# Kernel tuning notes

Measured on AMD Instinct MI355X. Metric: run time of the kernel, lower is better.

## Reference

```python
import jax, jax.numpy as jnp
import numpy as np

N_ROI = 2000
N_CLASSES = 21            # VOC: 20 fg + background (class 0 skipped in suppression)
IMG_H, IMG_W = 600.0, 800.0
NMS_THRESH = 0.3          # use_preset('evaluate')
SCORE_THRESH = 0.05
LOC_MEAN = jnp.array([0.0, 0.0, 0.0, 0.0], jnp.float32)
LOC_STD = jnp.array([0.1, 0.1, 0.2, 0.2], jnp.float32)


def setup_inputs() -> dict:
    key = jax.random.key(0)
    k1, k2, k3, k4 = jax.random.split(key, 4)
    # rois in (y1, x1, y2, x2) with y2 > y1, x2 > x1, inside the image
    yx1 = jax.random.uniform(k1, (N_ROI, 2), jnp.float32) * jnp.array([IMG_H * 0.8, IMG_W * 0.8])
    hw = jax.random.uniform(k2, (N_ROI, 2), jnp.float32) * jnp.array([IMG_H * 0.3, IMG_W * 0.3]) + 8.0
    rois = jnp.concatenate([yx1, yx1 + hw], axis=1)
    roi_cls_locs = jax.random.normal(k3, (N_ROI, N_CLASSES * 4), jnp.float32) * 0.5
    roi_scores = jax.random.normal(k4, (N_ROI, N_CLASSES), jnp.float32) * 2.0
    scale = jnp.ones((1,), jnp.float32)
    return {"rois": rois, "roi_cls_locs": roi_cls_locs, "roi_scores": roi_scores, "scale": scale}


def loc2bbox(src_bbox, loc):
    # src_bbox, loc: [..., 4] in (y1, x1, y2, x2) / (dy, dx, dh, dw)
    h = src_bbox[..., 2] - src_bbox[..., 0]
    w = src_bbox[..., 3] - src_bbox[..., 1]
    cy = src_bbox[..., 0] + 0.5 * h
    cx = src_bbox[..., 1] + 0.5 * w
    dy, dx, dh, dw = loc[..., 0], loc[..., 1], loc[..., 2], loc[..., 3]
    ncy = dy * h + cy
    ncx = dx * w + cx
    nh = jnp.exp(dh) * h
    nw = jnp.exp(dw) * w
    return jnp.stack([ncy - 0.5 * nh, ncx - 0.5 * nw, ncy + 0.5 * nh, ncx + 0.5 * nw], axis=-1)


def pairwise_iou(b):
    # b: [N, 4] -> [N, N]
    area = (b[:, 2] - b[:, 0]) * (b[:, 3] - b[:, 1])
    ty = jnp.maximum(b[:, None, 0], b[None, :, 0])
    tx = jnp.maximum(b[:, None, 1], b[None, :, 1])
    by = jnp.minimum(b[:, None, 2], b[None, :, 2])
    bx = jnp.minimum(b[:, None, 3], b[None, :, 3])
    inter = jnp.clip(by - ty, 0.0) * jnp.clip(bx - tx, 0.0)
    return inter / (area[:, None] + area[None, :] - inter + 1e-12)


def nms_keep(boxes, scores, valid):
    # Fixed-shape NMS: returns boolean keep mask in original order.
    n = boxes.shape[0]
    order = jnp.argsort(-jnp.where(valid, scores, -jnp.inf))
    b = boxes[order]
    v = valid[order]
    iou = pairwise_iou(b)  # [N, N]
    idx = jnp.arange(n)

    def body(i, keep):
        sup = keep[i] & (iou[i] > NMS_THRESH) & (idx > i)
        return keep & ~sup

    keep_sorted = jax.lax.fori_loop(0, n, body, v)
    return jnp.zeros(n, bool).at[order].set(keep_sorted)


def reference(rois, roi_cls_locs, roi_scores, scale):
    n, c = roi_scores.shape
    mean = jnp.tile(LOC_MEAN, c)
    std = jnp.tile(LOC_STD, c)
    locs = (roi_cls_locs * std + mean).reshape(n, c, 4)
    src = jnp.broadcast_to(rois[:, None, :], (n, c, 4))
    bboxes = loc2bbox(src, locs)  # [N, C, 4]
    original_size = jnp.array([IMG_H, IMG_W], jnp.float32) / scale[0]
    bboxes = jnp.stack([
        jnp.clip(bboxes[..., 0], 0.0, original_size[0]),
        jnp.clip(bboxes[..., 1], 0.0, original_size[1]),
        jnp.clip(bboxes[..., 2], 0.0, original_size[0]),
        jnp.clip(bboxes[..., 3], 0.0, original_size[1]),
    ], axis=-1)
    prob = jax.nn.softmax(roi_scores, axis=-1)

    # drop background class 0; class-major layout [C-1, N, ...]
    boxes_c = jnp.transpose(bboxes[:, 1:, :], (1, 0, 2))  # [C-1, N, 4]
    probs_c = prob[:, 1:].T                                # [C-1, N]
    valid = probs_c > SCORE_THRESH
    keep = jax.vmap(nms_keep)(boxes_c, probs_c, valid)     # [C-1, N] bool

    out5 = jnp.where(keep[..., None],
                     jnp.concatenate([boxes_c, probs_c[..., None]], axis=-1),
                     0.0)                                  # [C-1, N, 5]
    labels = jnp.broadcast_to(jnp.arange(c - 1, dtype=jnp.int32)[:, None], keep.shape)
    return out5, keep, labels
```

## Files before the change

kernel.cpp:

```cpp
#include <hip/hip_runtime.h>
#include <math.h>

#define NROI 2000
#define NCLS 21
#define NFG  20
#define NPAD 2048
#define NTOT (NFG * NROI)

#define OFF_PROBS   0u
#define OFF_SIDX    160000u
#define OFF_SPROB   323840u
#define OFF_SBOX    487680u
#define OFF_VC      1143040u
#define OFF_MASK    1143296u

typedef unsigned long long u64;

__global__ void k_prob(const float* __restrict__ scores,
                       float* __restrict__ probs) {
#pragma clang fp contract(off)
    int n = blockIdx.x * blockDim.x + threadIdx.x;
    if (n >= NROI) return;
    float s[NCLS];
    float m = -__builtin_inff();
#pragma unroll
    for (int k = 0; k < NCLS; ++k) {
        s[k] = scores[n * NCLS + k];
        m = fmaxf(m, s[k]);
    }
    float sum = 0.0f;
#pragma unroll
    for (int k = 0; k < NCLS; ++k) sum += expf(s[k] - m);
#pragma unroll
    for (int c = 0; c < NFG; ++c)
        probs[c * NROI + n] = expf(s[c + 1] - m) / sum;
}

#define CSW(A,B,UP) { u64 lo_ = x[A] < x[B] ? x[A] : x[B]; \
                      u64 hi_ = x[A] < x[B] ? x[B] : x[A]; \
                      x[A] = (UP) ? lo_ : hi_; x[B] = (UP) ? hi_ : lo_; }

__global__ void __launch_bounds__(256) k_sort(const float* __restrict__ rois,
                                              const float* __restrict__ locs,
                                              const float* __restrict__ probs,
                                              const float* __restrict__ scale,
                                              int* __restrict__ sidx,
                                              float* __restrict__ sprob,
                                              float4* __restrict__ sbox,
                                              int* __restrict__ Vc,
                                              float* __restrict__ out) {
#pragma clang fp contract(off)
    int c = blockIdx.x;
    int cc = c + 1;
    int t = threadIdx.x;
    __shared__ u64 a[NPAD];
    __shared__ int vcount;
    if (t == 0) vcount = 0;

    u64 x[8];
    int cnt = 0;
#pragma unroll
    for (int i = 0; i < 8; ++i) {
        int e = 8 * t + i;
        unsigned int u;
        if (e < NROI) {
            float pr = probs[c * NROI + e];
            bool valid = pr > 0.05f;
            cnt += valid ? 1 : 0;
            float key = valid ? pr : -__builtin_inff();
            u = __float_as_uint(key);
        } else {
            u = __float_as_uint(-__builtin_inff());
        }
        u ^= (u >> 31) ? 0xFFFFFFFFu : 0x80000000u;
        x[i] = ((u64)(~u) << 32) | (unsigned int)e;
    }
    __syncthreads();
    if (cnt) atomicAdd(&vcount, cnt);

    {
        float4 z4 = make_float4(0.f, 0.f, 0.f, 0.f);
        float4* o5v = (float4*)out + (size_t)c * (NROI * 5 / 4);
        for (int i = t; i < NROI * 5 / 4; i += 256) o5v[i] = z4;
        float lc = (float)c;
        for (int i = t; i < NROI; i += 256) {
            out[(size_t)5 * NTOT + c * NROI + i] = 0.0f;
            out[(size_t)6 * NTOT + c * NROI + i] = lc;
        }
    }

    CSW(0,1,true)  CSW(2,3,false) CSW(4,5,true)  CSW(6,7,false)
    CSW(0,2,true)  CSW(1,3,true)  CSW(4,6,false) CSW(5,7,false)
    CSW(0,1,true)  CSW(2,3,true)  CSW(4,5,false) CSW(6,7,false)
    {
        bool up = (t & 1) == 0;
        CSW(0,4,up) CSW(1,5,up) CSW(2,6,up) CSW(3,7,up)
        CSW(0,2,up) CSW(1,3,up) CSW(4,6,up) CSW(5,7,up)
        CSW(0,1,up) CSW(2,3,up) CSW(4,5,up) CSW(6,7,up)
    }
    for (unsigned int k = 16; k <= NPAD; k <<= 1) {
        bool up = (((unsigned int)(8 * t)) & k) == 0;
        for (unsigned int j = k >> 1; j >= 8; j >>= 1) {
            if (j >= 512) {
                __syncthreads();
#pragma unroll
                for (int i = 0; i < 8; ++i) a[8 * t + i] = x[i];
                __syncthreads();
                bool lower = ((t & (j >> 3)) == 0);
                bool takeMin = (up == lower);
#pragma unroll
                for (int i = 0; i < 8; ++i) {
                    u64 y = a[(8 * t + i) ^ j];
                    u64 mn = x[i] < y ? x[i] : y;
                    u64 mx = x[i] < y ? y : x[i];
                    x[i] = takeMin ? mn : mx;
                }
            } else {
                int lm = (int)(j >> 3);
                bool lower = ((t & lm) == 0);
                bool takeMin = (up == lower);
#pragma unroll
                for (int i = 0; i < 8; ++i) {
                    u64 y = __shfl_xor(x[i], lm, 64);
                    u64 mn = x[i] < y ? x[i] : y;
                    u64 mx = x[i] < y ? y : x[i];
                    x[i] = takeMin ? mn : mx;
                }
            }
        }
        CSW(0,4,up) CSW(1,5,up) CSW(2,6,up) CSW(3,7,up)
        CSW(0,2,up) CSW(1,3,up) CSW(4,6,up) CSW(5,7,up)
        CSW(0,1,up) CSW(2,3,up) CSW(4,5,up) CSW(6,7,up)
    }

    float sc = scale[0];
    float oh = 600.0f / sc, ow = 800.0f / sc;
#pragma unroll
    for (int i = 0; i < 8; ++i) {
        int slot = 8 * t + i;
        u64 p = x[i];
        int orig = (int)(p & 0xFFFFFFFFu);
        sidx[c * NPAD + slot] = orig;
        unsigned int m_ = ~(unsigned int)(p >> 32);
        unsigned int b_ = (m_ & 0x80000000u) ? (m_ ^ 0x80000000u) : ~m_;
        sprob[c * NPAD + slot] = __uint_as_float(b_);

        float4 bb = make_float4(0.f, 0.f, 0.f, 0.f);
        if (orig < NROI) {
            const float4 rr = *(const float4*)(rois + (size_t)orig * 4);
            const float4 ll = *(const float4*)(locs + (size_t)orig * (NCLS * 4) + cc * 4);
            float h = rr.z - rr.x, w = rr.w - rr.y;
            float cy = rr.x + 0.5f * h, cx = rr.y + 0.5f * w;
            float dy = ll.x * 0.1f, dx = ll.y * 0.1f;
            float dh = ll.z * 0.2f, dw = ll.w * 0.2f;
            float ncy = dy * h + cy;
            float ncx = dx * w + cx;
            float nh = expf(dh) * h;
            float nw = expf(dw) * w;
            float b0 = ncy - 0.5f * nh;
            float b1 = ncx - 0.5f * nw;
            float b2 = ncy + 0.5f * nh;
            float b3 = ncx + 0.5f * nw;
            bb.x = fminf(fmaxf(b0, 0.0f), oh);
            bb.y = fminf(fmaxf(b1, 0.0f), ow);
            bb.z = fminf(fmaxf(b2, 0.0f), oh);
            bb.w = fminf(fmaxf(b3, 0.0f), ow);
        }
        sbox[c * NPAD + slot] = bb;
    }
    __syncthreads();
    if (t == 0) Vc[c] = vcount;
}

__global__ void __launch_bounds__(512) k_mask(const float4* __restrict__ sbox,
                                              const int* __restrict__ Vc,
                                              u64* __restrict__ mask) {
#pragma clang fp contract(off)
    int c = blockIdx.y;
    int V = Vc[c];
    int jb = blockIdx.x;
    int j0 = jb << 6;
    if (j0 >= V) return;
    int tid = threadIdx.x;
    int lane = tid & 63;
    int wv = tid >> 6;
    int rmax = min(V, j0 + 64);
    int smax = j0 + 64;

    __shared__ float4 lb[NPAD];
    const float4* sb = sbox + c * NPAD;
    for (int i = tid; i < smax; i += 512) lb[i] = sb[i];
    __syncthreads();

    int j = j0 + lane;
    float4 cb = lb[j];
    float areaC = (cb.z - cb.x) * (cb.w - cb.y);
    u64* mrow = mask + (size_t)(c * NPAD) * 32 + jb;

    for (int r0 = wv * 8; r0 < rmax; r0 += 64) {
#pragma unroll
        for (int k = 0; k < 8; ++k) {
            int r = r0 + k;
            bool act = r < rmax;
            float4 rb = lb[act ? r : 0];
            float areaR = (rb.z - rb.x) * (rb.w - rb.y);
            float ty = fmaxf(rb.x, cb.x);
            float tx = fmaxf(rb.y, cb.y);
            float by = fminf(rb.z, cb.z);
            float bx = fminf(rb.w, cb.w);
            float ih = fmaxf(by - ty, 0.0f);
            float iw = fmaxf(bx - tx, 0.0f);
            float inter = ih * iw;
            float denom = ((areaR + areaC) - inter) + 1e-12f;
            float iou = inter / denom;
            u64 bits = __ballot((j > r) && (iou > 0.3f));
            if (act && lane == 0) mrow[(size_t)r * 32] = bits;
        }
    }
}

__global__ void __launch_bounds__(64, 1) k_scan(const int* __restrict__ sidx,
                                                const float* __restrict__ sprob,
                                                const float4* __restrict__ sbox,
                                                const int* __restrict__ Vc,
                                                const u64* __restrict__ mask,
                                                float* __restrict__ out) {
    int c = blockIdx.x;
    int V = Vc[c];
    if (V <= 0) return;
    int lane = threadIdx.x;
    int w = lane & 31;
    const u64* mbase = mask + (size_t)c * NPAD * 32;

    int ntiles = (V + 63) >> 6;
    u64 remv = 0;
    u64 d = mbase[(size_t)lane * 32 + 0];

    for (int t = 0; t < ntiles; ++t) {
        u64 dn = 0;
        if (t + 1 < ntiles)
            dn = mbase[(size_t)(64 * (t + 1) + lane) * 32 + (t + 1)];

        int r = 64 * t + lane;
        bool act = r < V;
        int ri = act ? r : 0;
        int orig = sidx[c * NPAD + ri];
        float pr = sprob[c * NPAD + ri];
        float4 bb = sbox[c * NPAD + ri];

        u64 pf[64];
        const u64* rp = mbase + (size_t)(64 * t) * 32 + w;
#pragma unroll
        for (int j = 0; j < 64; ++j) pf[j] = rp[(size_t)j * 32];

        u64 rv = __shfl(remv, t);
        int rem = V - 64 * t;
        u64 validm = (rem >= 64) ? ~0ULL : ((1ULL << rem) - 1ULL);
        u64 cur = (~rv) & validm;
        u64 kept = 0;
        while (cur) {
            int j = __ffsll((u64)cur) - 1;
            kept |= 1ULL << j;
            cur &= ~__shfl(d, j);
            cur &= ~(1ULL << j);
        }

        u64 acc = 0;
#pragma unroll
        for (int j = 0; j < 64; ++j) {
            u64 sel = 0ULL - ((kept >> j) & 1ULL);
            acc |= pf[j] & sel;
        }
        remv |= acc;

        if (act && ((kept >> lane) & 1ULL)) {
            size_t to = (size_t)c * NROI + orig;
            float* o5 = out + to * 5;
            o5[0] = bb.x; o5[1] = bb.y; o5[2] = bb.z; o5[3] = bb.w; o5[4] = pr;
            out[(size_t)5 * NTOT + to] = 1.0f;
        }
        d = dn;
    }
}

extern "C" void kernel_launch(void* const* d_in, const int* in_sizes, int n_in,
                              void* d_out, int out_size, void* d_ws, size_t ws_size,
                              hipStream_t stream) {
    const float* rois   = (const float*)d_in[0];
    const float* locs   = (const float*)d_in[1];
    const float* scores = (const float*)d_in[2];
    const float* scale  = (const float*)d_in[3];
    float* out = (float*)d_out;

    char* ws = (char*)d_ws;
    float*  probs = (float*)(ws + OFF_PROBS);
    int*    sidx  = (int*)(ws + OFF_SIDX);
    float*  sprob = (float*)(ws + OFF_SPROB);
    float4* sbox  = (float4*)(ws + OFF_SBOX);
    int*    Vc    = (int*)(ws + OFF_VC);
    u64*    mask  = (u64*)(ws + OFF_MASK);

    hipLaunchKernelGGL(k_prob, dim3(32), dim3(64), 0, stream,
                       scores, probs);
    hipLaunchKernelGGL(k_sort, dim3(NFG), dim3(256), 0, stream,
                       rois, locs, probs, scale, sidx, sprob, sbox, Vc, out);
    hipLaunchKernelGGL(k_mask, dim3(32, NFG), dim3(512), 0, stream,
                       sbox, Vc, mask);
    hipLaunchKernelGGL(k_scan, dim3(NFG), dim3(64), 0, stream,
                       sidx, sprob, sbox, Vc, mask, out);
}
```

Before: 87.65 us.

## Fuse sort, IoU mask and NMS scan into one per-class kernel

Merges the sort, mask and scan kernels into a single 1024-thread block per class. Sorted keys and decoded boxes stay in LDS, and the IoU bitmask is stored as a packed upper triangle, in LDS when it fits and in global memory otherwise. This removes two launches and the global round trips for the sorted index, probability, box and mask buffers. The cost is that the mask computation now runs on only 20 workgroups instead of up to 640, so per-class parallelism drops, and the large LDS footprint allows one block per CU.

```diff
diff --git a/kernel.cpp b/kernel.cpp
--- a/kernel.cpp
+++ b/kernel.cpp
@@ -7,12 +7,12 @@
 #define NPAD 2048
 #define NTOT (NFG * NROI)
 
+#define NT_LDS_MAX 19
+#define TRI_LDS_WORDS 12160
+#define TRI_GBL_WORDS 33792
+
 #define OFF_PROBS   0u
-#define OFF_SIDX    160000u
-#define OFF_SPROB   323840u
-#define OFF_SBOX    487680u
-#define OFF_VC      1143040u
-#define OFF_MASK    1143296u
+#define OFF_GMASK   163840u
 
 typedef unsigned long long u64;
 
@@ -40,54 +40,53 @@
                       u64 hi_ = x[A] < x[B] ? x[B] : x[A]; \
                       x[A] = (UP) ? lo_ : hi_; x[B] = (UP) ? hi_ : lo_; }
 
-__global__ void __launch_bounds__(256) k_sort(const float* __restrict__ rois,
-                                              const float* __restrict__ locs,
-                                              const float* __restrict__ probs,
-                                              const float* __restrict__ scale,
-                                              int* __restrict__ sidx,
-                                              float* __restrict__ sprob,
-                                              float4* __restrict__ sbox,
-                                              int* __restrict__ Vc,
-                                              float* __restrict__ out) {
+__device__ __forceinline__ int tri_base(int T, int NT) {
+    return 64 * (T * NT - (T * (T - 1)) / 2);
+}
+
+__global__ void __launch_bounds__(1024, 1)
+k_mega(const float* __restrict__ rois,
+       const float* __restrict__ locs,
+       const float* __restrict__ probs,
+       const float* __restrict__ scale,
+       u64* __restrict__ gmask,
+       float* __restrict__ out) {
 #pragma clang fp contract(off)
     int c = blockIdx.x;
     int cc = c + 1;
     int t = threadIdx.x;
+
     __shared__ u64 a[NPAD];
+    __shared__ float4 lb[NPAD];
+    __shared__ u64 s_tri[TRI_LDS_WORDS];
     __shared__ int vcount;
     if (t == 0) vcount = 0;
 
     u64 x[8];
     int cnt = 0;
-#pragma unroll
-    for (int i = 0; i < 8; ++i) {
-        int e = 8 * t + i;
-        unsigned int u;
-        if (e < NROI) {
-            float pr = probs[c * NROI + e];
-            bool valid = pr > 0.05f;
-            cnt += valid ? 1 : 0;
-            float key = valid ? pr : -__builtin_inff();
-            u = __float_as_uint(key);
-        } else {
-            u = __float_as_uint(-__builtin_inff());
-        }
-        u ^= (u >> 31) ? 0xFFFFFFFFu : 0x80000000u;
-        x[i] = ((u64)(~u) << 32) | (unsigned int)e;
+    if (t < 256) {
+#pragma unroll
+        for (int i = 0; i < 8; ++i) {
+            int e = 8 * t + i;
+            unsigned int u;
+            if (e < NROI) {
+                float pr = probs[c * NROI + e];
+                bool valid = pr > 0.05f;
+                cnt += valid ? 1 : 0;
+                float key = valid ? pr : -__builtin_inff();
+                u = __float_as_uint(key);
+            } else {
+                u = __float_as_uint(-__builtin_inff());
+            }
+            u ^= (u >> 31) ? 0xFFFFFFFFu : 0x80000000u;
+            x[i] = ((u64)(~u) << 32) | (unsigned int)e;
+        }
+    } else {
+#pragma unroll
+        for (int i = 0; i < 8; ++i) x[i] = 0;
     }
     __syncthreads();
     if (cnt) atomicAdd(&vcount, cnt);
-
-    {
-        float4 z4 = make_float4(0.f, 0.f, 0.f, 0.f);
-        float4* o5v = (float4*)out + (size_t)c * (NROI * 5 / 4);
-        for (int i = t; i < NROI * 5 / 4; i += 256) o5v[i] = z4;
-        float lc = (float)c;
-        for (int i = t; i < NROI; i += 256) {
-            out[(size_t)5 * NTOT + c * NROI + i] = 0.0f;
-            out[(size_t)6 * NTOT + c * NROI + i] = lc;
-        }
-    }
 
     CSW(0,1,true)  CSW(2,3,false) CSW(4,5,true)  CSW(6,7,false)
     CSW(0,2,true)  CSW(1,3,true)  CSW(4,6,false) CSW(5,7,false)
@@ -103,17 +102,21 @@
         for (unsigned int j = k >> 1; j >= 8; j >>= 1) {
             if (j >= 512) {
                 __syncthreads();
-#pragma unroll
-                for (int i = 0; i < 8; ++i) a[8 * t + i] = x[i];
+                if (t < 256) {
+#pragma unroll
+                    for (int i = 0; i < 8; ++i) a[8 * t + i] = x[i];
+                }
                 __syncthreads();
-                bool lower = ((t & (j >> 3)) == 0);
-                bool takeMin = (up == lower);
-#pragma unroll
-                for (int i = 0; i < 8; ++i) {
-                    u64 y = a[(8 * t + i) ^ j];
-                    u64 mn = x[i] < y ? x[i] : y;
-                    u64 mx = x[i] < y ? y : x[i];
-                    x[i] = takeMin ? mn : mx;
+                if (t < 256) {
+                    bool lower = ((t & (j >> 3)) == 0);
+                    bool takeMin = (up == lower);
+#pragma unroll
+                    for (int i = 0; i < 8; ++i) {
+                        u64 y = a[(8 * t + i) ^ j];
+                        u64 mn = x[i] < y ? x[i] : y;
+                        u64 mx = x[i] < y ? y : x[i];
+                        x[i] = takeMin ? mn : mx;
+                    }
                 }
             } else {
                 int lm = (int)(j >> 3);
@@ -132,154 +135,147 @@
         CSW(0,2,up) CSW(1,3,up) CSW(4,6,up) CSW(5,7,up)
         CSW(0,1,up) CSW(2,3,up) CSW(4,5,up) CSW(6,7,up)
     }
-
-    float sc = scale[0];
-    float oh = 600.0f / sc, ow = 800.0f / sc;
-#pragma unroll
-    for (int i = 0; i < 8; ++i) {
-        int slot = 8 * t + i;
-        u64 p = x[i];
-        int orig = (int)(p & 0xFFFFFFFFu);
-        sidx[c * NPAD + slot] = orig;
-        unsigned int m_ = ~(unsigned int)(p >> 32);
-        unsigned int b_ = (m_ & 0x80000000u) ? (m_ ^ 0x80000000u) : ~m_;
-        sprob[c * NPAD + slot] = __uint_as_float(b_);
-
-        float4 bb = make_float4(0.f, 0.f, 0.f, 0.f);
-        if (orig < NROI) {
-            const float4 rr = *(const float4*)(rois + (size_t)orig * 4);
-            const float4 ll = *(const float4*)(locs + (size_t)orig * (NCLS * 4) + cc * 4);
-            float h = rr.z - rr.x, w = rr.w - rr.y;
-            float cy = rr.x + 0.5f * h, cx = rr.y + 0.5f * w;
-            float dy = ll.x * 0.1f, dx = ll.y * 0.1f;
-            float dh = ll.z * 0.2f, dw = ll.w * 0.2f;
-            float ncy = dy * h + cy;
-            float ncx = dx * w + cx;
-            float nh = expf(dh) * h;
-            float nw = expf(dw) * w;
-            float b0 = ncy - 0.5f * nh;
-            float b1 = ncx - 0.5f * nw;
-            float b2 = ncy + 0.5f * nh;
-            float b3 = ncx + 0.5f * nw;
-            bb.x = fminf(fmaxf(b0, 0.0f), oh);
-            bb.y = fminf(fmaxf(b1, 0.0f), ow);
-            bb.z = fminf(fmaxf(b2, 0.0f), oh);
-            bb.w = fminf(fmaxf(b3, 0.0f), ow);
-        }
-        sbox[c * NPAD + slot] = bb;
-    }
-    __syncthreads();
-    if (t == 0) Vc[c] = vcount;
-}
-
-__global__ void __launch_bounds__(512) k_mask(const float4* __restrict__ sbox,
-                                              const int* __restrict__ Vc,
-                                              u64* __restrict__ mask) {
-#pragma clang fp contract(off)
-    int c = blockIdx.y;
-    int V = Vc[c];
-    int jb = blockIdx.x;
-    int j0 = jb << 6;
-    if (j0 >= V) return;
-    int tid = threadIdx.x;
-    int lane = tid & 63;
-    int wv = tid >> 6;
-    int rmax = min(V, j0 + 64);
-    int smax = j0 + 64;
-
-    __shared__ float4 lb[NPAD];
-    const float4* sb = sbox + c * NPAD;
-    for (int i = tid; i < smax; i += 512) lb[i] = sb[i];
-    __syncthreads();
-
-    int j = j0 + lane;
-    float4 cb = lb[j];
-    float areaC = (cb.z - cb.x) * (cb.w - cb.y);
-    u64* mrow = mask + (size_t)(c * NPAD) * 32 + jb;
-
-    for (int r0 = wv * 8; r0 < rmax; r0 += 64) {
-#pragma unroll
-        for (int k = 0; k < 8; ++k) {
-            int r = r0 + k;
-            bool act = r < rmax;
-            float4 rb = lb[act ? r : 0];
-            float areaR = (rb.z - rb.x) * (rb.w - rb.y);
-            float ty = fmaxf(rb.x, cb.x);
-            float tx = fmaxf(rb.y, cb.y);
-            float by = fminf(rb.z, cb.z);
-            float bx = fminf(rb.w, cb.w);
-            float ih = fmaxf(by - ty, 0.0f);
-            float iw = fmaxf(bx - tx, 0.0f);
-            float inter = ih * iw;
-            float denom = ((areaR + areaC) - inter) + 1e-12f;
-            float iou = inter / denom;
-            u64 bits = __ballot((j > r) && (iou > 0.3f));
-            if (act && lane == 0) mrow[(size_t)r * 32] = bits;
-        }
-    }
-}
-
-__global__ void __launch_bounds__(64, 1) k_scan(const int* __restrict__ sidx,
-                                                const float* __restrict__ sprob,
-                                                const float4* __restrict__ sbox,
-                                                const int* __restrict__ Vc,
-                                                const u64* __restrict__ mask,
-                                                float* __restrict__ out) {
-    int c = blockIdx.x;
-    int V = Vc[c];
-    if (V <= 0) return;
-    int lane = threadIdx.x;
-    int w = lane & 31;
-    const u64* mbase = mask + (size_t)c * NPAD * 32;
-
-    int ntiles = (V + 63) >> 6;
-    u64 remv = 0;
-    u64 d = mbase[(size_t)lane * 32 + 0];
-
-    for (int t = 0; t < ntiles; ++t) {
-        u64 dn = 0;
-        if (t + 1 < ntiles)
-            dn = mbase[(size_t)(64 * (t + 1) + lane) * 32 + (t + 1)];
-
-        int r = 64 * t + lane;
-        bool act = r < V;
-        int ri = act ? r : 0;
-        int orig = sidx[c * NPAD + ri];
-        float pr = sprob[c * NPAD + ri];
-        float4 bb = sbox[c * NPAD + ri];
-
-        u64 pf[64];
-        const u64* rp = mbase + (size_t)(64 * t) * 32 + w;
-#pragma unroll
-        for (int j = 0; j < 64; ++j) pf[j] = rp[(size_t)j * 32];
-
-        u64 rv = __shfl(remv, t);
-        int rem = V - 64 * t;
-        u64 validm = (rem >= 64) ? ~0ULL : ((1ULL << rem) - 1ULL);
-        u64 cur = (~rv) & validm;
-        u64 kept = 0;
-        while (cur) {
-            int j = __ffsll((u64)cur) - 1;
-            kept |= 1ULL << j;
-            cur &= ~__shfl(d, j);
-            cur &= ~(1ULL << j);
-        }
-
-        u64 acc = 0;
-#pragma unroll
-        for (int j = 0; j < 64; ++j) {
-            u64 sel = 0ULL - ((kept >> j) & 1ULL);
-            acc |= pf[j] & sel;
-        }
-        remv |= acc;
-
-        if (act && ((kept >> lane) & 1ULL)) {
-            size_t to = (size_t)c * NROI + orig;
-            float* o5 = out + to * 5;
-            o5[0] = bb.x; o5[1] = bb.y; o5[2] = bb.z; o5[3] = bb.w; o5[4] = pr;
-            out[(size_t)5 * NTOT + to] = 1.0f;
-        }
-        d = dn;
+    __syncthreads();
+    if (t < 256) {
+#pragma unroll
+        for (int i = 0; i < 8; ++i) a[8 * t + i] = x[i];
+    }
+    __syncthreads();
+
+    int V = vcount;
+    int NT = (V + 63) >> 6;
+    bool use_lds = (NT <= NT_LDS_MAX);
+    u64* tri = use_lds ? (u64*)s_tri : (gmask + (size_t)c * TRI_GBL_WORDS);
+
+    {
+        float sc = scale[0];
+        float oh = 600.0f / sc, ow = 800.0f / sc;
+#pragma unroll
+        for (int q = 0; q < 2; ++q) {
+            int slot = t + q * 1024;
+            u64 p = a[slot];
+            int orig = (int)(p & 0xFFFFFFFFu);
+            float4 bb = make_float4(0.f, 0.f, 0.f, 0.f);
+            if (orig < NROI) {
+                const float4 rr = *(const float4*)(rois + (size_t)orig * 4);
+                const float4 ll = *(const float4*)(locs + (size_t)orig * (NCLS * 4) + cc * 4);
+                float h = rr.z - rr.x, w = rr.w - rr.y;
+                float cy = rr.x + 0.5f * h, cx = rr.y + 0.5f * w;
+                float dy = ll.x * 0.1f, dx = ll.y * 0.1f;
+                float dh = ll.z * 0.2f, dw = ll.w * 0.2f;
+                float ncy = dy * h + cy;
+                float ncx = dx * w + cx;
+                float nh = expf(dh) * h;
+                float nw = expf(dw) * w;
+                float b0 = ncy - 0.5f * nh;
+                float b1 = ncx - 0.5f * nw;
+                float b2 = ncy + 0.5f * nh;
+                float b3 = ncx + 0.5f * nw;
+                bb.x = fminf(fmaxf(b0, 0.0f), oh);
+                bb.y = fminf(fmaxf(b1, 0.0f), ow);
+                bb.z = fminf(fmaxf(b2, 0.0f), oh);
+                bb.w = fminf(fmaxf(b3, 0.0f), ow);
+            }
+            lb[slot] = bb;
+        }
+        float4 z4 = make_float4(0.f, 0.f, 0.f, 0.f);
+        float4* o5v = (float4*)out + (size_t)c * (NROI * 5 / 4);
+        for (int i = t; i < NROI * 5 / 4; i += 1024) o5v[i] = z4;
+        float lc = (float)c;
+        for (int i = t; i < NROI; i += 1024) {
+            out[(size_t)5 * NTOT + c * NROI + i] = 0.0f;
+            out[(size_t)6 * NTOT + c * NROI + i] = lc;
+        }
+    }
+    __syncthreads();
+
+    {
+        int lane = t & 63;
+        int wv = t >> 6;
+        int u = 0;
+        for (int rt = 0; rt < NT; ++rt) {
+            for (int jb = rt; jb < NT; ++jb, ++u) {
+                if ((u & 15) != wv) continue;
+                int j = (jb << 6) + lane;
+                float4 cb = lb[j];
+                float areaC = (cb.z - cb.x) * (cb.w - cb.y);
+                int r0 = rt << 6;
+                int rend = min(V, r0 + 64);
+                int stride = NT - rt;
+                int bidx = tri_base(rt, NT) + (jb - rt);
+#pragma unroll 4
+                for (int r = r0; r < rend; ++r) {
+                    float4 rb = lb[r];
+                    float areaR = (rb.z - rb.x) * (rb.w - rb.y);
+                    float ty = fmaxf(rb.x, cb.x);
+                    float tx = fmaxf(rb.y, cb.y);
+                    float by = fminf(rb.z, cb.z);
+                    float bx = fminf(rb.w, cb.w);
+                    float ih = fmaxf(by - ty, 0.0f);
+                    float iw = fmaxf(bx - tx, 0.0f);
+                    float inter = ih * iw;
+                    float denom = ((areaR + areaC) - inter) + 1e-12f;
+                    float iou = inter / denom;
+                    u64 bits = __ballot((j > r) && (iou > 0.3f));
+                    if (lane == 0) tri[bidx + (r - r0) * stride] = bits;
+                }
+            }
+        }
+    }
+    __syncthreads();
+
+    if (t < 64 && V > 0) {
+        int lane = t;
+        int w = lane & 31;
+        u64 remv = 0;
+        for (int T = 0; T < NT; ++T) {
+            int stride = NT - T;
+            int tb = tri_base(T, NT);
+            u64 d = tri[tb + lane * stride];
+
+            u64 rv = __shfl(remv, T);
+            int rem = V - 64 * T;
+            u64 validm = (rem >= 64) ? ~0ULL : ((1ULL << rem) - 1ULL);
+            u64 cur = (~rv) & validm;
+            u64 kept = 0;
+            while (cur) {
+                int j = __ffsll((u64)cur) - 1;
+                kept |= 1ULL << j;
+                cur &= ~__shfl(d, j);
+                cur &= ~(1ULL << j);
+            }
+
+            if (w >= T && w < NT) {
+                int bidx = tb + (w - T);
+                u64 acc = 0;
+#pragma unroll 1
+                for (int jj = 0; jj < 64; jj += 32) {
+                    u64 pf[32];
+#pragma unroll
+                    for (int q = 0; q < 32; ++q) pf[q] = tri[bidx + (jj + q) * stride];
+#pragma unroll
+                    for (int q = 0; q < 32; ++q) {
+                        u64 sel = 0ULL - ((kept >> (jj + q)) & 1ULL);
+                        acc |= pf[q] & sel;
+                    }
+                }
+                remv |= acc;
+            }
+
+            int r = 64 * T + lane;
+            if (r < V && ((kept >> lane) & 1ULL)) {
+                u64 p = a[r];
+                int orig = (int)(p & 0xFFFFFFFFu);
+                unsigned int m_ = ~(unsigned int)(p >> 32);
+                unsigned int b_ = (m_ & 0x80000000u) ? (m_ ^ 0x80000000u) : ~m_;
+                float pr = __uint_as_float(b_);
+                float4 bb = lb[r];
+                size_t to = (size_t)c * NROI + orig;
+                float* o5 = out + to * 5;
+                o5[0] = bb.x; o5[1] = bb.y; o5[2] = bb.z; o5[3] = bb.w; o5[4] = pr;
+                out[(size_t)5 * NTOT + to] = 1.0f;
+            }
+        }
     }
 }
 
@@ -293,19 +289,11 @@
     float* out = (float*)d_out;
 
     char* ws = (char*)d_ws;
-    float*  probs = (float*)(ws + OFF_PROBS);
-    int*    sidx  = (int*)(ws + OFF_SIDX);
-    float*  sprob = (float*)(ws + OFF_SPROB);
-    float4* sbox  = (float4*)(ws + OFF_SBOX);
-    int*    Vc    = (int*)(ws + OFF_VC);
-    u64*    mask  = (u64*)(ws + OFF_MASK);
+    float* probs = (float*)(ws + OFF_PROBS);
+    u64*   gmask = (u64*)(ws + OFF_GMASK);
 
     hipLaunchKernelGGL(k_prob, dim3(32), dim3(64), 0, stream,
                        scores, probs);
-    hipLaunchKernelGGL(k_sort, dim3(NFG), dim3(256), 0, stream,
-                       rois, locs, probs, scale, sidx, sprob, sbox, Vc, out);
-    hipLaunchKernelGGL(k_mask, dim3(32, NFG), dim3(512), 0, stream,
-                       sbox, Vc, mask);
-    hipLaunchKernelGGL(k_scan, dim3(NFG), dim3(64), 0, stream,
-                       sidx, sprob, sbox, Vc, mask, out);
-}
+    hipLaunchKernelGGL(k_mega, dim3(NFG), dim3(1024), 0, stream,
+                       rois, locs, probs, scale, gmask, out);
+}
```

After: 117.6 us. +34.2%, slower.
